# Kernel tuning notes

Measured on AMD Instinct MI355X. Metric: run time of the kernel, lower is better.

## Reference

```python
import jax, jax.numpy as jnp
import numpy as np

NCONST = 100
NFEATS = 16
NCLASS = 5
NEFF = 6
NDYN = 6
BN_EPS = 1e-3  # keras BatchNormalization default epsilon


def _edge_indices(nconst):
    # itertools.product order, skipping self-pairs, matching _build_relation_matrices
    recv, send = [], []
    for i in range(nconst):
        for j in range(nconst):
            if i != j:
                recv.append(i)
                send.append(j)
    return np.asarray(recv, np.int32), np.asarray(send, np.int32)


def setup_inputs() -> dict:
    key = jax.random.key(0)
    ks = jax.random.split(key, 16)

    def w(k, shape, fan_in):
        return (jax.random.normal(k, shape, jnp.float32) / np.sqrt(fan_in)).astype(jnp.float32)

    inp = {
        "x": jax.random.normal(ks[0], (512, NCONST, NFEATS), jnp.float32),
        # batchnorm (inference-mode) params over the feature axis
        "bn_gamma": jnp.ones((NFEATS,), jnp.float32),
        "bn_beta": jnp.zeros((NFEATS,), jnp.float32),
        "bn_mean": jnp.zeros((NFEATS,), jnp.float32),
        "bn_var": jnp.ones((NFEATS,), jnp.float32),
        # fr: pointwise Conv1D == dense over last dim; 2*nfeats -> 30 -> 15 -> 6
        "fr_w1": w(ks[1], (2 * NFEATS, 30), 2 * NFEATS), "fr_b1": jnp.zeros((30,), jnp.float32),
        "fr_w2": w(ks[2], (30, 15), 30), "fr_b2": jnp.zeros((15,), jnp.float32),
        "fr_w3": w(ks[3], (15, NEFF), 15), "fr_b3": jnp.zeros((NEFF,), jnp.float32),
        # fo: (nfeats + neffects) -> 45 -> 22 -> 6
        "fo_w1": w(ks[4], (NFEATS + NEFF, 45), NFEATS + NEFF), "fo_b1": jnp.zeros((45,), jnp.float32),
        "fo_w2": w(ks[5], (45, 22), 45), "fo_b2": jnp.zeros((22,), jnp.float32),
        "fo_w3": w(ks[6], (22, NDYN), 22), "fo_b3": jnp.zeros((NDYN,), jnp.float32),
        # fc: ndyn -> 48 -> nclasses (softmax)
        "fc_w1": w(ks[7], (NDYN, 48), NDYN), "fc_b1": jnp.zeros((48,), jnp.float32),
        "fc_w2": w(ks[8], (48, NCLASS), 48), "fc_b2": jnp.zeros((NCLASS,), jnp.float32),
    }
    return inp


def reference(x, bn_gamma, bn_beta, bn_mean, bn_var,
              fr_w1, fr_b1, fr_w2, fr_b2, fr_w3, fr_b3,
              fo_w1, fo_b1, fo_w2, fo_b2, fo_w3, fo_b3,
              fc_w1, fc_b1, fc_w2, fc_b2):
    nconst = x.shape[1]
    recv_idx, send_idx = _edge_indices(nconst)  # static, shape (nedges,)

    # BatchNormalization (inference) over the feature axis: (B, N, F)
    xb = (x - bn_mean) * jax.lax.rsqrt(bn_var + BN_EPS) * bn_gamma + bn_beta

    # One-hot relation matmuls are exact gathers: (B, E, F) each.
    # Concat order matches Concatenate(axis=1)([receiver, sender]) pre-permute.
    fr_in = jnp.concatenate([xb[:, recv_idx, :], xb[:, send_idx, :]], axis=-1)  # (B, E, 2F)

    h = jax.nn.relu(fr_in @ fr_w1 + fr_b1)
    h = jax.nn.relu(h @ fr_w2 + fr_b2)
    effects = jax.nn.relu(h @ fr_w3 + fr_b3)  # (B, E, neff)

    # Multiplying by receiver_matrix^T is a scatter-add of edge effects to receiver nodes.
    agg = jnp.zeros((x.shape[0], nconst, effects.shape[-1]), effects.dtype)
    agg = agg.at[:, recv_idx, :].add(effects)  # (B, N, neff)

    fo_in = jnp.concatenate([xb, agg], axis=-1)  # (B, N, F + neff)
    d = jax.nn.relu(fo_in @ fo_w1 + fo_b1)
    d = jax.nn.relu(d @ fo_w2 + fo_b2)
    d = jax.nn.relu(d @ fo_w3 + fo_b3)  # (B, N, ndyn)

    fc_in = jnp.sum(d, axis=1)  # summation=True -> (B, ndyn)
    h = jax.nn.relu(fc_in @ fc_w1 + fc_b1)
    logits = h @ fc_w2 + fc_b2
    return jax.nn.softmax(logits, axis=-1)  # (B, nclasses)
```

## Files before the change

### kernel.cpp

```cpp
#include <hip/hip_runtime.h>
#include <math.h>

#define NCONST 100
#define NF     16
#define BLK    1024
#define NWAVES 16

typedef _Float16 f16x8 __attribute__((ext_vector_type(8)));
typedef float    f32x4 __attribute__((ext_vector_type(4)));

__global__ __launch_bounds__(BLK, 4) void convint_fused(
    const float* __restrict__ x,
    const float* __restrict__ bn_g, const float* __restrict__ bn_b,
    const float* __restrict__ bn_m, const float* __restrict__ bn_v,
    const float* __restrict__ frw1, const float* __restrict__ frb1,
    const float* __restrict__ frw2, const float* __restrict__ frb2,
    const float* __restrict__ frw3, const float* __restrict__ frb3,
    const float* __restrict__ fow1, const float* __restrict__ fob1,
    const float* __restrict__ fow2, const float* __restrict__ fob2,
    const float* __restrict__ fow3, const float* __restrict__ fob3,
    const float* __restrict__ fcw1, const float* __restrict__ fcb1,
    const float* __restrict__ fcw2, const float* __restrict__ fcb2,
    float* __restrict__ out)
{
    __shared__ float xbn[NCONST][NF];
    __shared__ float upool[6704];
    __shared__ float aggF[NCONST * 9];
    __shared__ float fcin[8];
    __shared__ float hfc[48];
    __shared__ float logits[8];

    _Float16* const Prh = (_Float16*)upool;
    _Float16* const Psh = (_Float16*)(upool + 2000);
    float (*const foh1)[45] = (float (*)[45])upool;
    float (*const foh2)[22] = (float (*)[22])(upool + 4500);

    const int b   = blockIdx.x;
    const int tid = threadIdx.x;
    const float* xb = x + (size_t)b * (NCONST * NF);

    for (int idx = tid; idx < NCONST * NF; idx += BLK) {
        int f = idx & 15;
        float sc = rsqrtf(bn_v[f] + 1e-3f) * bn_g[f];
        xbn[idx >> 4][f] = (xb[idx] - bn_m[f]) * sc + bn_b[f];
    }
    if (tid < 8) fcin[tid] = 0.f;
    for (int idx = tid; idx < NCONST * 10; idx += BLK) {
        int n = idx / 10, kk = idx - n * 10;
        Prh[n * 40 + 30 + kk] = (_Float16)0.f;
        Psh[n * 40 + 30 + kk] = (_Float16)0.f;
    }
    __syncthreads();

    for (int idx = tid; idx < 6000; idx += BLK) {
        int n   = idx / 60;
        int rem = idx - n * 60;
        int sel = (rem >= 30) ? 1 : 0;
        int o   = rem - sel * 30;
        const float* w = frw1 + (sel * 16) * 30 + o;
        float acc = sel ? 0.f : frb1[o];
        #pragma unroll
        for (int f = 0; f < 16; ++f) acc = fmaf(xbn[n][f], w[f * 30], acc);
        if (sel) Psh[n * 40 + o] = (_Float16)acc;
        else     Prh[n * 40 + o] = (_Float16)acc;
    }
    __syncthreads();

    {
        const int l  = tid & 63;
        const int wv = tid >> 6;
        const int o  = l & 15;
        const int kb = l >> 4;

        f16x8 bf1, bf2;
        #pragma unroll
        for (int m = 0; m < 8; ++m) {
            int k = kb * 8 + m;
            bf1[m] = (k < 30 && o < 15) ? (_Float16)frw2[k * 15 + o] : (_Float16)0.f;
            bf2[m] = (k < 15 && o < 6)  ? (_Float16)frw3[k * 6 + o]  : (_Float16)0.f;
        }
        float b2r[4];
        #pragma unroll
        for (int r = 0; r < 4; ++r) {
            int o2 = kb * 4 + r;
            b2r[r] = (o2 < 15) ? frb2[o2] : 0.f;
        }
        const float b3l = (o < 6) ? frb3[o] : 0.f;
        const int kb1 = kb & 1;
        const int perm0 = (o + 16 * (((kb1 * 8) + 0) >> 2)) << 2;
        const int perm1 = (o + 16 * (((kb1 * 8) + 2) >> 2)) << 2;
        const int perm2 = (o + 16 * (((kb1 * 8) + 4) >> 2)) << 2;
        const int perm3 = (o + 16 * (((kb1 * 8) + 6) >> 2)) << 2;
        f32x4 cz; cz[0] = 0.f; cz[1] = 0.f; cz[2] = 0.f; cz[3] = 0.f;

        for (int i = wv; i < NCONST; i += NWAVES) {
            const f16x8 pri = *(const f16x8*)(Prh + i * 40 + kb * 8);
            f32x4 racc = cz;
            #pragma unroll 1
            for (int tb = 0; tb < 7; ++tb) {
                int si = tb * 16 + o;
                int j  = i + 1 + si;
                if (j >= 100) j -= 100;
                if (j >= 100) j -= 100;
                f16x8 ps = *(const f16x8*)(Psh + j * 40 + kb * 8);
                f16x8 h1;
                #pragma unroll
                for (int m = 0; m < 8; ++m) {
                    _Float16 v = (_Float16)(pri[m] + ps[m]);
                    h1[m] = (v > (_Float16)0.f) ? v : (_Float16)0.f;
                }
                f32x4 c1 = __builtin_amdgcn_mfma_f32_16x16x32_f16(bf1, h1, cz, 0, 0, 0);
                union { unsigned u; _Float16 h[2]; } pk0, pk1;
                pk0.h[0] = (_Float16)fmaxf(c1[0] + b2r[0], 0.f);
                pk0.h[1] = (_Float16)fmaxf(c1[1] + b2r[1], 0.f);
                pk1.h[0] = (_Float16)fmaxf(c1[2] + b2r[2], 0.f);
                pk1.h[1] = (_Float16)fmaxf(c1[3] + b2r[3], 0.f);
                union { int w[4]; f16x8 v; } a2u;
                a2u.w[0] = __builtin_amdgcn_ds_bpermute(perm0, (int)pk0.u);
                a2u.w[1] = __builtin_amdgcn_ds_bpermute(perm1, (int)pk1.u);
                a2u.w[2] = __builtin_amdgcn_ds_bpermute(perm2, (int)pk0.u);
                a2u.w[3] = __builtin_amdgcn_ds_bpermute(perm3, (int)pk1.u);
                f32x4 c2 = __builtin_amdgcn_mfma_f32_16x16x32_f16(a2u.v, bf2, cz, 0, 0, 0);
                #pragma unroll
                for (int r = 0; r < 4; ++r) {
                    int row = kb * 4 + r;
                    float v = fmaxf(c2[r] + b3l, 0.f);
                    racc[r] += (tb * 16 + row < 99) ? v : 0.f;
                }
            }
            float s2 = racc[0] + racc[1] + racc[2] + racc[3];
            s2 += __shfl_xor(s2, 16);
            s2 += __shfl_xor(s2, 32);
            if (kb == 0 && o < 6) aggF[i * 9 + o] = s2;
        }
    }
    __syncthreads();

    for (int idx = tid; idx < NCONST * 45; idx += BLK) {
        int n = idx / 45, o = idx - n * 45;
        float acc = fob1[o];
        #pragma unroll
        for (int k = 0; k < 16; ++k) acc = fmaf(xbn[n][k], fow1[k*45+o], acc);
        #pragma unroll
        for (int k = 0; k < 6; ++k)  acc = fmaf(aggF[n*9+k], fow1[(16+k)*45+o], acc);
        foh1[n][o] = fmaxf(acc, 0.f);
    }
    __syncthreads();

    for (int idx = tid; idx < NCONST * 22; idx += BLK) {
        int n = idx / 22, o = idx - n * 22;
        float acc = fob2[o];
        #pragma unroll
        for (int k = 0; k < 45; ++k) acc = fmaf(foh1[n][k], fow2[k*22+o], acc);
        foh2[n][o] = fmaxf(acc, 0.f);
    }
    __syncthreads();

    for (int idx = tid; idx < NCONST * 6; idx += BLK) {
        int n = idx / 6, c = idx - n * 6;
        float acc = fob3[c];
        #pragma unroll
        for (int k = 0; k < 22; ++k) acc = fmaf(foh2[n][k], fow3[k*6+c], acc);
        atomicAdd(&fcin[c], fmaxf(acc, 0.f));
    }
    __syncthreads();

    if (tid < 48) {
        float acc = fcb1[tid];
        #pragma unroll
        for (int k = 0; k < 6; ++k) acc = fmaf(fcin[k], fcw1[k*48 + tid], acc);
        hfc[tid] = fmaxf(acc, 0.f);
    }
    __syncthreads();
    if (tid < 5) {
        float acc = fcb2[tid];
        #pragma unroll
        for (int k = 0; k < 48; ++k) acc = fmaf(hfc[k], fcw2[k*5 + tid], acc);
        logits[tid] = acc;
    }
    __syncthreads();
    if (tid == 0) {
        float m = logits[0];
        #pragma unroll
        for (int c = 1; c < 5; ++c) m = fmaxf(m, logits[c]);
        float ex[5], sum = 0.f;
        #pragma unroll
        for (int c = 0; c < 5; ++c) { ex[c] = __expf(logits[c] - m); sum += ex[c]; }
        float inv = 1.f / sum;
        #pragma unroll
        for (int c = 0; c < 5; ++c) out[(size_t)b * 5 + c] = ex[c] * inv;
    }
}

extern "C" void kernel_launch(void* const* d_in, const int* in_sizes, int n_in,
                              void* d_out, int out_size, void* d_ws, size_t ws_size,
                              hipStream_t stream) {
    const float* x     = (const float*)d_in[0];
    const float* bn_g  = (const float*)d_in[1];
    const float* bn_b  = (const float*)d_in[2];
    const float* bn_m  = (const float*)d_in[3];
    const float* bn_v  = (const float*)d_in[4];
    const float* frw1  = (const float*)d_in[5];
    const float* frb1  = (const float*)d_in[6];
    const float* frw2  = (const float*)d_in[7];
    const float* frb2  = (const float*)d_in[8];
    const float* frw3  = (const float*)d_in[9];
    const float* frb3  = (const float*)d_in[10];
    const float* fow1  = (const float*)d_in[11];
    const float* fob1  = (const float*)d_in[12];
    const float* fow2  = (const float*)d_in[13];
    const float* fob2  = (const float*)d_in[14];
    const float* fow3  = (const float*)d_in[15];
    const float* fob3  = (const float*)d_in[16];
    const float* fcw1  = (const float*)d_in[17];
    const float* fcb1  = (const float*)d_in[18];
    const float* fcw2  = (const float*)d_in[19];
    const float* fcb2  = (const float*)d_in[20];

    const int B = in_sizes[0] / (NCONST * NF);

    convint_fused<<<dim3(B), dim3(BLK), 0, stream>>>(
        x, bn_g, bn_b, bn_m, bn_v,
        frw1, frb1, frw2, frb2, frw3, frb3,
        fow1, fob1, fow2, fob2, fow3, fob3,
        fcw1, fcb1, fcw2, fcb2,
        (float*)d_out);
}
```

Measured before the change: 68.63 us.

## Vectorize LDS reads, compute four fr layer-1 outputs per thread, raise min blocks

Raises the launch-bounds minimum-blocks hint from 4 to 8. The fr layer-1 projection now computes four outputs per thread from one float4 read of the node's features, using float2 weight loads and packed f16 stores. The fo layers pad their shared arrays to 48 and 24 columns (aggF to 8) so rows can be read as float4 instead of scalars. The pairwise loop is unrolled by 2 and does the f16 add as a vector op. The aim is fewer LDS and global load instructions and fewer redundant loads of xbn. The higher blocks hint may cap registers, which could cause spills.

```diff
diff --git a/kernel.cpp b/kernel.cpp
--- a/kernel.cpp
+++ b/kernel.cpp
@@ -7,9 +7,11 @@
 #define NWAVES 16
 
 typedef _Float16 f16x8 __attribute__((ext_vector_type(8)));
+typedef _Float16 f16x4 __attribute__((ext_vector_type(4)));
+typedef _Float16 f16x2 __attribute__((ext_vector_type(2)));
 typedef float    f32x4 __attribute__((ext_vector_type(4)));
 
-__global__ __launch_bounds__(BLK, 4) void convint_fused(
+__global__ __launch_bounds__(BLK, 8) void convint_fused(
     const float* __restrict__ x,
     const float* __restrict__ bn_g, const float* __restrict__ bn_b,
     const float* __restrict__ bn_m, const float* __restrict__ bn_v,
@@ -24,16 +26,16 @@
     float* __restrict__ out)
 {
     __shared__ float xbn[NCONST][NF];
-    __shared__ float upool[6704];
-    __shared__ float aggF[NCONST * 9];
+    __shared__ float upool[7200];
+    __shared__ float aggF[NCONST * 8];
     __shared__ float fcin[8];
     __shared__ float hfc[48];
     __shared__ float logits[8];
 
     _Float16* const Prh = (_Float16*)upool;
     _Float16* const Psh = (_Float16*)(upool + 2000);
-    float (*const foh1)[45] = (float (*)[45])upool;
-    float (*const foh2)[22] = (float (*)[22])(upool + 4500);
+    float (*const foh1)[48] = (float (*)[48])upool;
+    float (*const foh2)[24] = (float (*)[24])(upool + 4800);
 
     const int b   = blockIdx.x;
     const int tid = threadIdx.x;
@@ -52,17 +54,49 @@
     }
     __syncthreads();
 
-    for (int idx = tid; idx < 6000; idx += BLK) {
-        int n   = idx / 60;
-        int rem = idx - n * 60;
-        int sel = (rem >= 30) ? 1 : 0;
-        int o   = rem - sel * 30;
-        const float* w = frw1 + (sel * 16) * 30 + o;
-        float acc = sel ? 0.f : frb1[o];
-        #pragma unroll
-        for (int f = 0; f < 16; ++f) acc = fmaf(xbn[n][f], w[f * 30], acc);
-        if (sel) Psh[n * 40 + o] = (_Float16)acc;
-        else     Prh[n * 40 + o] = (_Float16)acc;
+    for (int idx = tid; idx < 1600; idx += BLK) {
+        int n   = idx >> 4;
+        int rem = idx & 15;
+        int sel = rem >> 3;
+        int oq  = rem & 7;
+        int o0  = oq * 4;
+
+        float xs[16];
+        {
+            const float4* xv = (const float4*)(&xbn[n][0]);
+            float4 x0 = xv[0], x1 = xv[1], x2 = xv[2], x3 = xv[3];
+            xs[0]=x0.x; xs[1]=x0.y; xs[2]=x0.z; xs[3]=x0.w;
+            xs[4]=x1.x; xs[5]=x1.y; xs[6]=x1.z; xs[7]=x1.w;
+            xs[8]=x2.x; xs[9]=x2.y; xs[10]=x2.z; xs[11]=x2.w;
+            xs[12]=x3.x; xs[13]=x3.y; xs[14]=x3.z; xs[15]=x3.w;
+        }
+        float acc0 = sel ? 0.f : frb1[o0 + 0];
+        float acc1 = sel ? 0.f : frb1[o0 + 1];
+        float acc2 = (!sel && oq < 7) ? frb1[o0 + 2] : 0.f;
+        float acc3 = (!sel && oq < 7) ? frb1[o0 + 3] : 0.f;
+        const int wcol2 = (oq < 7) ? o0 + 2 : 28;
+        const float* wbase = frw1 + (sel ? 16 * 30 : 0);
+        #pragma unroll
+        for (int f = 0; f < 16; ++f) {
+            const float* wr = wbase + f * 30;
+            float2 wa = *(const float2*)(wr + o0);
+            float2 wb = *(const float2*)(wr + wcol2);
+            acc0 = fmaf(xs[f], wa.x, acc0);
+            acc1 = fmaf(xs[f], wa.y, acc1);
+            acc2 = fmaf(xs[f], wb.x, acc2);
+            acc3 = fmaf(xs[f], wb.y, acc3);
+        }
+        _Float16* dst = (sel ? Psh : Prh) + n * 40 + o0;
+        if (oq < 7) {
+            f16x4 hv;
+            hv[0] = (_Float16)acc0; hv[1] = (_Float16)acc1;
+            hv[2] = (_Float16)acc2; hv[3] = (_Float16)acc3;
+            *(f16x4*)dst = hv;
+        } else {
+            f16x2 hv;
+            hv[0] = (_Float16)acc0; hv[1] = (_Float16)acc1;
+            *(f16x2*)dst = hv;
+        }
     }
     __syncthreads();
 
@@ -96,19 +130,19 @@
         for (int i = wv; i < NCONST; i += NWAVES) {
             const f16x8 pri = *(const f16x8*)(Prh + i * 40 + kb * 8);
             f32x4 racc = cz;
-            #pragma unroll 1
+            #pragma unroll 2
             for (int tb = 0; tb < 7; ++tb) {
                 int si = tb * 16 + o;
                 int j  = i + 1 + si;
                 if (j >= 100) j -= 100;
                 if (j >= 100) j -= 100;
                 f16x8 ps = *(const f16x8*)(Psh + j * 40 + kb * 8);
+                f16x8 v = pri + ps;
                 f16x8 h1;
                 #pragma unroll
-                for (int m = 0; m < 8; ++m) {
-                    _Float16 v = (_Float16)(pri[m] + ps[m]);
-                    h1[m] = (v > (_Float16)0.f) ? v : (_Float16)0.f;
-                }
+                for (int m = 0; m < 8; ++m)
+                    h1[m] = (v[m] > (_Float16)0.f) ? v[m] : (_Float16)0.f;
+
                 f32x4 c1 = __builtin_amdgcn_mfma_f32_16x16x32_f16(bf1, h1, cz, 0, 0, 0);
                 union { unsigned u; _Float16 h[2]; } pk0, pk1;
                 pk0.h[0] = (_Float16)fmaxf(c1[0] + b2r[0], 0.f);
@@ -124,14 +158,14 @@
                 #pragma unroll
                 for (int r = 0; r < 4; ++r) {
                     int row = kb * 4 + r;
-                    float v = fmaxf(c2[r] + b3l, 0.f);
-                    racc[r] += (tb * 16 + row < 99) ? v : 0.f;
+                    float vv = fmaxf(c2[r] + b3l, 0.f);
+                    racc[r] += (tb * 16 + row < 99) ? vv : 0.f;
                 }
             }
             float s2 = racc[0] + racc[1] + racc[2] + racc[3];
             s2 += __shfl_xor(s2, 16);
             s2 += __shfl_xor(s2, 32);
-            if (kb == 0 && o < 6) aggF[i * 9 + o] = s2;
+            if (kb == 0 && o < 6) aggF[i * 8 + o] = s2;
         }
     }
     __syncthreads();
@@ -139,10 +173,23 @@
     for (int idx = tid; idx < NCONST * 45; idx += BLK) {
         int n = idx / 45, o = idx - n * 45;
         float acc = fob1[o];
-        #pragma unroll
-        for (int k = 0; k < 16; ++k) acc = fmaf(xbn[n][k], fow1[k*45+o], acc);
-        #pragma unroll
-        for (int k = 0; k < 6; ++k)  acc = fmaf(aggF[n*9+k], fow1[(16+k)*45+o], acc);
+        const float4* xv = (const float4*)(&xbn[n][0]);
+        #pragma unroll
+        for (int q = 0; q < 4; ++q) {
+            float4 xq = xv[q];
+            acc = fmaf(xq.x, fow1[(4*q+0)*45 + o], acc);
+            acc = fmaf(xq.y, fow1[(4*q+1)*45 + o], acc);
+            acc = fmaf(xq.z, fow1[(4*q+2)*45 + o], acc);
+            acc = fmaf(xq.w, fow1[(4*q+3)*45 + o], acc);
+        }
+        const float4 a0 = *(const float4*)(&aggF[n * 8]);
+        const float2 a1 = *(const float2*)(&aggF[n * 8 + 4]);
+        acc = fmaf(a0.x, fow1[16*45 + o], acc);
+        acc = fmaf(a0.y, fow1[17*45 + o], acc);
+        acc = fmaf(a0.z, fow1[18*45 + o], acc);
+        acc = fmaf(a0.w, fow1[19*45 + o], acc);
+        acc = fmaf(a1.x, fow1[20*45 + o], acc);
+        acc = fmaf(a1.y, fow1[21*45 + o], acc);
         foh1[n][o] = fmaxf(acc, 0.f);
     }
     __syncthreads();
@@ -150,8 +197,16 @@
     for (int idx = tid; idx < NCONST * 22; idx += BLK) {
         int n = idx / 22, o = idx - n * 22;
         float acc = fob2[o];
-        #pragma unroll
-        for (int k = 0; k < 45; ++k) acc = fmaf(foh1[n][k], fow2[k*22+o], acc);
+        const float4* hv = (const float4*)(&foh1[n][0]);
+        #pragma unroll
+        for (int q = 0; q < 11; ++q) {
+            float4 h4 = hv[q];
+            acc = fmaf(h4.x, fow2[(4*q+0)*22 + o], acc);
+            acc = fmaf(h4.y, fow2[(4*q+1)*22 + o], acc);
+            acc = fmaf(h4.z, fow2[(4*q+2)*22 + o], acc);
+            acc = fmaf(h4.w, fow2[(4*q+3)*22 + o], acc);
+        }
+        acc = fmaf(foh1[n][44], fow2[44*22 + o], acc);
         foh2[n][o] = fmaxf(acc, 0.f);
     }
     __syncthreads();
@@ -159,8 +214,17 @@
     for (int idx = tid; idx < NCONST * 6; idx += BLK) {
         int n = idx / 6, c = idx - n * 6;
         float acc = fob3[c];
-        #pragma unroll
-        for (int k = 0; k < 22; ++k) acc = fmaf(foh2[n][k], fow3[k*6+c], acc);
+        const float4* hv = (const float4*)(&foh2[n][0]);
+        #pragma unroll
+        for (int q = 0; q < 5; ++q) {
+            float4 h4 = hv[q];
+            acc = fmaf(h4.x, fow3[(4*q+0)*6 + c], acc);
+            acc = fmaf(h4.y, fow3[(4*q+1)*6 + c], acc);
+            acc = fmaf(h4.z, fow3[(4*q+2)*6 + c], acc);
+            acc = fmaf(h4.w, fow3[(4*q+3)*6 + c], acc);
+        }
+        acc = fmaf(foh2[n][20], fow3[20*6 + c], acc);
+        acc = fmaf(foh2[n][21], fow3[21*6 + c], acc);
         atomicAdd(&fcin[c], fmaxf(acc, 0.f));
     }
     __syncthreads();
```

Result: no change. 68.30 us (-0.5%).
